# Kernel optimization log

Hardware: AMD Instinct MI355X
Metric: run time of the kernel (lower is better)

## Reference

```python
import jax, jax.numpy as jnp
import numpy as np

N = 100000   # nodes per type (author == paper count here)
E = 800000   # edges per edge type
D = 128      # input feature dim
HID = 128    # hidden_channels
OUT = 64     # out_channels
L = 2        # num_layers


def setup_inputs() -> dict:
    key = jax.random.key(0)
    ks = jax.random.split(key, 14)
    x_author = jax.random.normal(ks[0], (N, D), jnp.float32)
    x_paper = jax.random.normal(ks[1], (N, D), jnp.float32)
    edge_ap = jnp.stack([
        jax.random.randint(ks[2], (E,), 0, N),
        jax.random.randint(ks[3], (E,), 0, N),
    ]).astype(jnp.int32)  # [2,E] author->paper (src,dst)
    # paper->author: ensure every paper id appears as a source so the
    # meta-path conversion keeps all E edges (static shape under jit)
    pa_src = jnp.concatenate([jnp.arange(N), jax.random.randint(ks[4], (E - N,), 0, N)]).astype(jnp.int32)
    pa_dst = jax.random.randint(ks[5], (E,), 0, N).astype(jnp.int32)
    edge_pa = jnp.stack([pa_src, pa_dst])
    perm = jax.random.permutation(ks[6], N).astype(jnp.int32)  # DGI corruption
    s = 0.05
    # SAGEConv params: [layer, edge_type] with edge_type 0 = (author->paper), 1 = (paper->author)
    sage_Wl = jax.random.normal(ks[7], (L, 2, HID, D), jnp.float32) * s   # neighbor lin
    sage_Wr = jax.random.normal(ks[8], (L, 2, HID, D), jnp.float32) * s   # root lin
    sage_b = jnp.zeros((L, 2, HID), jnp.float32)
    # GATConv (heads=1) params
    gat_W = jax.random.normal(ks[9], (OUT, HID), jnp.float32) * s
    gat_att_src = jax.random.normal(ks[10], (OUT,), jnp.float32) * s
    gat_att_dst = jax.random.normal(ks[11], (OUT,), jnp.float32) * s
    gat_b = jnp.zeros((OUT,), jnp.float32)
    prelu_a = jnp.asarray(0.25, jnp.float32)
    return dict(x_author=x_author, x_paper=x_paper, sage_Wl=sage_Wl, sage_Wr=sage_Wr,
                sage_b=sage_b, gat_W=gat_W, gat_att_src=gat_att_src, gat_att_dst=gat_att_dst,
                gat_b=gat_b, prelu_a=prelu_a, edge_ap=edge_ap, edge_pa=edge_pa, perm=perm)


def _sage(x_src, x_dst, src, dst, Wl, Wr, b, n_dst):
    # SAGEConv: mean-aggregate neighbor feats, lin_l(agg) + lin_r(root) + bias
    agg = jax.ops.segment_sum(x_src[src], dst, num_segments=n_dst)       # [n_dst, D]
    cnt = jax.ops.segment_sum(jnp.ones((src.shape[0],), x_src.dtype), dst, num_segments=n_dst)
    mean = agg / jnp.maximum(cnt, 1.0)[:, None]
    return mean @ Wl.T + x_dst @ Wr.T + b


def _gat_prelu(feat, src, dst, W, a_src, a_dst, b, prelu_a, n):
    # GATConv heads=1 (self loops already appended by caller) + PReLU
    h = feat @ W.T                                                        # [n, OUT]
    e = jax.nn.leaky_relu((h @ a_src)[src] + (h @ a_dst)[dst], 0.2)       # [E']
    m = jax.ops.segment_max(e, dst, num_segments=n)
    ex = jnp.exp(e - m[dst])
    den = jax.ops.segment_sum(ex, dst, num_segments=n)
    coef = ex / den[dst]
    out = jax.ops.segment_sum(coef[:, None] * h[src], dst, num_segments=n) + b
    return jnp.where(out >= 0, out, prelu_a * out)


def reference(x_author, x_paper, sage_Wl, sage_Wr, sage_b, gat_W, gat_att_src,
              gat_att_dst, gat_b, prelu_a, edge_ap, edge_pa, perm):
    # Original loop feeds xx_dict into every layer, so only the LAST layer's
    # output survives; and only x_dict['author'] is consumed downstream.
    l = L - 1
    h_author = jax.nn.leaky_relu(
        _sage(x_paper, x_author, edge_pa[0], edge_pa[1],
              sage_Wl[l, 1], sage_Wr[l, 1], sage_b[l, 1], N), 0.01)
    # meta-path author->author edges (paper mapped via last-write paper->author dict)
    p2a = jnp.zeros((N,), jnp.int32).at[edge_pa[0]].set(edge_pa[1])
    self_loop = jnp.arange(N, dtype=jnp.int32)  # GATConv add_self_loops=True
    meta_src = jnp.concatenate([edge_ap[0], self_loop])
    meta_dst = jnp.concatenate([p2a[edge_ap[1]], self_loop])
    pos = _gat_prelu(h_author, meta_src, meta_dst, gat_W, gat_att_src, gat_att_dst, gat_b, prelu_a, N)
    neg = _gat_prelu(h_author[perm], meta_src, meta_dst, gat_W, gat_att_src, gat_att_dst, gat_b, prelu_a, N)
    summary = jnp.mean(pos, axis=0)
    return pos, neg, summary
```

## Files before the change

### kernel.cpp

```cpp
#include <hip/hip_runtime.h>
#include <stdint.h>

#define NN 100000
#define EE 800000
#define DD 128
#define HH 128
#define OO 64

#define SPA 40
#define SME 112
#define CPAD 16

typedef __attribute__((ext_vector_type(8))) short short8v;
typedef __attribute__((ext_vector_type(4))) float f32x4;

__device__ __forceinline__ unsigned short f2bf(float f) {
    union { float f; unsigned int u; } v; v.f = f;
    unsigned int u = v.u;
    u = (u + 0x7fffu + ((u >> 16) & 1u)) >> 16;
    return (unsigned short)u;
}
__device__ __forceinline__ float bf2f(unsigned short b) {
    union { unsigned int u; float f; } v; v.u = ((unsigned int)b) << 16;
    return v.f;
}

__global__ __launch_bounds__(256) void k_cast(const float* __restrict__ x,
                                              unsigned short* __restrict__ xbf) {
    long i = (long)blockIdx.x * 256 + threadIdx.x;
    if (i >= (long)NN * DD / 4) return;
    float4 v = ((const float4*)x)[i];
    ushort4 w;
    w.x = f2bf(v.x); w.y = f2bf(v.y); w.z = f2bf(v.z); w.w = f2bf(v.w);
    ((ushort4*)xbf)[i] = w;
}

__global__ __launch_bounds__(256) void k_p2a_init(const int* __restrict__ pa_dst,
                                                  unsigned long long* __restrict__ p2a) {
    int s = blockIdx.x * 256 + threadIdx.x;
    if (s >= NN) return;
    p2a[s] = ((unsigned long long)(unsigned int)s << 32) | (unsigned int)pa_dst[s];
}

__global__ __launch_bounds__(256) void k_p2a(const int* __restrict__ pa_src,
                                             const int* __restrict__ pa_dst,
                                             unsigned long long* __restrict__ p2a,
                                             int* __restrict__ cnt_pa,
                                             int* __restrict__ col_pa) {
    int e = blockIdx.x * 256 + threadIdx.x;
    if (e >= EE) return;
    int s = pa_src[e], d = pa_dst[e];
    if (e >= NN) {
        unsigned long long key = ((unsigned long long)(unsigned int)e << 32) | (unsigned int)d;
        atomicMax(&p2a[s], key);
    }
    int pos = atomicAdd(&cnt_pa[d * CPAD], 1);
    if (pos < SPA) __builtin_nontemporal_store(s, &col_pa[d * SPA + pos]);
}

__global__ __launch_bounds__(256) void k_compact(const unsigned long long* __restrict__ p2a,
                                                 int* __restrict__ p2a32) {
    int s = blockIdx.x * 256 + threadIdx.x;
    if (s >= NN) return;
    p2a32[s] = (int)(p2a[s] & 0xffffffffull);
}

__global__ __launch_bounds__(256) void k_meta(const int* __restrict__ ap_src,
                                              const int* __restrict__ ap_dst,
                                              const int* __restrict__ p2a32,
                                              int* __restrict__ cnt_meta,
                                              int* __restrict__ col_meta) {
    int e = blockIdx.x * 256 + threadIdx.x;
    if (e >= EE) return;
    int d = p2a32[ap_dst[e]];
    int pos = atomicAdd(&cnt_meta[d * CPAD], 1);
    if (pos < SME) __builtin_nontemporal_store(ap_src[e], &col_meta[d * SME + pos]);
}

__global__ __launch_bounds__(256) void k_sage_gather(const int* __restrict__ cnt_pa,
                                                     const int* __restrict__ col_pa,
                                                     const unsigned short* __restrict__ xbf,
                                                     unsigned short* __restrict__ mean_bf) {
    long gid = (long)blockIdx.x * 256 + threadIdx.x;
    int d = (int)(gid >> 6);
    if (d >= NN) return;
    int lane = (int)(gid & 63);
    int dcnt = cnt_pa[d * CPAD];
    int deg = (dcnt > SPA) ? SPA : dcnt;
    const int* row = col_pa + d * SPA;
    float ax = 0.f, ay = 0.f;
    int i = 0;
    for (; i + 3 < deg; i += 4) {
        int s0 = row[i], s1 = row[i + 1], s2 = row[i + 2], s3 = row[i + 3];
        ushort2 v0 = ((const ushort2*)(xbf + (long)s0 * DD))[lane];
        ushort2 v1 = ((const ushort2*)(xbf + (long)s1 * DD))[lane];
        ushort2 v2 = ((const ushort2*)(xbf + (long)s2 * DD))[lane];
        ushort2 v3 = ((const ushort2*)(xbf + (long)s3 * DD))[lane];
        ax += (bf2f(v0.x) + bf2f(v1.x)) + (bf2f(v2.x) + bf2f(v3.x));
        ay += (bf2f(v0.y) + bf2f(v1.y)) + (bf2f(v2.y) + bf2f(v3.y));
    }
    for (; i < deg; ++i) {
        int s = row[i];
        ushort2 v = ((const ushort2*)(xbf + (long)s * DD))[lane];
        ax += bf2f(v.x);
        ay += bf2f(v.y);
    }
    float sc = 1.0f / fmaxf((float)dcnt, 1.0f);
    ushort2 w;
    w.x = f2bf(ax * sc);
    w.y = f2bf(ay * sc);
    ((ushort2*)(mean_bf + (long)d * DD))[lane] = w;
}

__global__ __launch_bounds__(256) void k_sagegemm(const unsigned short* __restrict__ mean_bf,
                                                  const float* __restrict__ xa,
                                                  const float* __restrict__ Wl,
                                                  const float* __restrict__ Wr,
                                                  const float* __restrict__ sb,
                                                  unsigned short* __restrict__ h) {
    __shared__ unsigned short wlds[2][HH * DD];
    int t = threadIdx.x;
    #pragma unroll
    for (int it = 0; it < 8; ++it) {
        int cid = t + it * 256;
        int o = cid >> 4, c = cid & 15;
        int boff = (o * 256 + c * 16) ^ ((o & 7) << 4);
        {
            const float4* p = (const float4*)(Wl + (long)o * DD + c * 8);
            float4 a = p[0], b = p[1];
            short8v w;
            w[0]=(short)f2bf(a.x); w[1]=(short)f2bf(a.y); w[2]=(short)f2bf(a.z); w[3]=(short)f2bf(a.w);
            w[4]=(short)f2bf(b.x); w[5]=(short)f2bf(b.y); w[6]=(short)f2bf(b.z); w[7]=(short)f2bf(b.w);
            *(short8v*)((char*)(&wlds[0][0]) + boff) = w;
        }
        {
            const float4* p = (const float4*)(Wr + (long)o * DD + c * 8);
            float4 a = p[0], b = p[1];
            short8v w;
            w[0]=(short)f2bf(a.x); w[1]=(short)f2bf(a.y); w[2]=(short)f2bf(a.z); w[3]=(short)f2bf(a.w);
            w[4]=(short)f2bf(b.x); w[5]=(short)f2bf(b.y); w[6]=(short)f2bf(b.z); w[7]=(short)f2bf(b.w);
            *(short8v*)((char*)(&wlds[1][0]) + boff) = w;
        }
    }
    __syncthreads();

    int wave = t >> 6, lane = t & 63;
    int rowbase = blockIdx.x * 128 + wave * 32;
    int lr = lane & 15;
    int kq = (lane >> 4) * 8;
    int r0 = rowbase + lr, r1 = r0 + 16;
    int cr0 = (r0 < NN) ? r0 : 0;
    int cr1 = (r1 < NN) ? r1 : 0;

    f32x4 acc[2][8];
    #pragma unroll
    for (int i = 0; i < 2; ++i)
        #pragma unroll
        for (int j = 0; j < 8; ++j) { f32x4 z = {0.f,0.f,0.f,0.f}; acc[i][j] = z; }

    #pragma unroll
    for (int k0 = 0; k0 < DD; k0 += 32) {
        int kk = k0 + kq;
        short8v am0 = *(const short8v*)(mean_bf + (long)cr0 * DD + kk);
        short8v am1 = *(const short8v*)(mean_bf + (long)cr1 * DD + kk);
        const float4* q0 = (const float4*)(xa + (long)cr0 * DD + kk);
        const float4* q1 = (const float4*)(xa + (long)cr1 * DD + kk);
        float4 a0 = q0[0], b0 = q0[1], a1 = q1[0], b1 = q1[1];
        short8v ax0, ax1;
        ax0[0]=(short)f2bf(a0.x); ax0[1]=(short)f2bf(a0.y); ax0[2]=(short)f2bf(a0.z); ax0[3]=(short)f2bf(a0.w);
        ax0[4]=(short)f2bf(b0.x); ax0[5]=(short)f2bf(b0.y); ax0[6]=(short)f2bf(b0.z); ax0[7]=(short)f2bf(b0.w);
        ax1[0]=(short)f2bf(a1.x); ax1[1]=(short)f2bf(a1.y); ax1[2]=(short)f2bf(a1.z); ax1[3]=(short)f2bf(a1.w);
        ax1[4]=(short)f2bf(b1.x); ax1[5]=(short)f2bf(b1.y); ax1[6]=(short)f2bf(b1.z); ax1[7]=(short)f2bf(b1.w);
        #pragma unroll
        for (int nb = 0; nb < 8; ++nb) {
            int o = nb * 16 + lr;
            int boff = (o * 256 + kk * 2) ^ ((o & 7) << 4);
            short8v bl = *(const short8v*)((const char*)(&wlds[0][0]) + boff);
            short8v br = *(const short8v*)((const char*)(&wlds[1][0]) + boff);
            acc[0][nb] = __builtin_amdgcn_mfma_f32_16x16x32_bf16(am0, bl, acc[0][nb], 0, 0, 0);
            acc[1][nb] = __builtin_amdgcn_mfma_f32_16x16x32_bf16(am1, bl, acc[1][nb], 0, 0, 0);
            acc[0][nb] = __builtin_amdgcn_mfma_f32_16x16x32_bf16(ax0, br, acc[0][nb], 0, 0, 0);
            acc[1][nb] = __builtin_amdgcn_mfma_f32_16x16x32_bf16(ax1, br, acc[1][nb], 0, 0, 0);
        }
    }
    int q = lane >> 4;
    #pragma unroll
    for (int rh = 0; rh < 2; ++rh) {
        #pragma unroll
        for (int nb = 0; nb < 8; ++nb) {
            int col = nb * 16 + lr;
            float bias = sb[col];
            #pragma unroll
            for (int r = 0; r < 4; ++r) {
                int row = rowbase + rh * 16 + q * 4 + r;
                if (row < NN) {
                    float v = acc[rh][nb][r] + bias;
                    v = (v >= 0.f) ? v : 0.01f * v;
                    h[(long)row * HH + col] = f2bf(v);
                }
            }
        }
    }
}

__global__ __launch_bounds__(256) void k_gatgemm(const unsigned short* __restrict__ h,
                                                 const float* __restrict__ Wg,
                                                 const float* __restrict__ asrc,
                                                 const float* __restrict__ adst,
                                                 unsigned short* __restrict__ hg,
                                                 float* __restrict__ al_s,
                                                 float* __restrict__ al_d) {
    __shared__ unsigned short wlds[OO * HH];
    int t = threadIdx.x;
    #pragma unroll
    for (int it = 0; it < 4; ++it) {
        int cid = t + it * 256;
        int o = cid >> 4, c = cid & 15;
        int boff = (o * 256 + c * 16) ^ ((o & 7) << 4);
        const float4* p = (const float4*)(Wg + (long)o * HH + c * 8);
        float4 a = p[0], b = p[1];
        short8v w;
        w[0]=(short)f2bf(a.x); w[1]=(short)f2bf(a.y); w[2]=(short)f2bf(a.z); w[3]=(short)f2bf(a.w);
        w[4]=(short)f2bf(b.x); w[5]=(short)f2bf(b.y); w[6]=(short)f2bf(b.z); w[7]=(short)f2bf(b.w);
        *(short8v*)((char*)(&wlds[0]) + boff) = w;
    }
    __syncthreads();

    int wave = t >> 6, lane = t & 63;
    int rowbase = blockIdx.x * 128 + wave * 32;
    int lr = lane & 15;
    int kq = (lane >> 4) * 8;
    int r0 = rowbase + lr, r1 = r0 + 16;
    int cr0 = (r0 < NN) ? r0 : 0;
    int cr1 = (r1 < NN) ? r1 : 0;

    f32x4 acc[2][4];
    #pragma unroll
    for (int i = 0; i < 2; ++i)
        #pragma unroll
        for (int j = 0; j < 4; ++j) { f32x4 z = {0.f,0.f,0.f,0.f}; acc[i][j] = z; }

    #pragma unroll
    for (int k0 = 0; k0 < HH; k0 += 32) {
        int kk = k0 + kq;
        short8v a0 = *(const short8v*)(h + (long)cr0 * HH + kk);
        short8v a1 = *(const short8v*)(h + (long)cr1 * HH + kk);
        #pragma unroll
        for (int nb = 0; nb < 4; ++nb) {
            int o = nb * 16 + lr;
            int boff = (o * 256 + kk * 2) ^ ((o & 7) << 4);
            short8v b = *(const short8v*)((const char*)(&wlds[0]) + boff);
            acc[0][nb] = __builtin_amdgcn_mfma_f32_16x16x32_bf16(a0, b, acc[0][nb], 0, 0, 0);
            acc[1][nb] = __builtin_amdgcn_mfma_f32_16x16x32_bf16(a1, b, acc[1][nb], 0, 0, 0);
        }
    }
    int q = lane >> 4;
    float a_s[4], a_d[4];
    #pragma unroll
    for (int nb = 0; nb < 4; ++nb) { a_s[nb] = asrc[nb * 16 + lr]; a_d[nb] = adst[nb * 16 + lr]; }
    #pragma unroll
    for (int rh = 0; rh < 2; ++rh) {
        float ss[4] = {0.f,0.f,0.f,0.f}, dd[4] = {0.f,0.f,0.f,0.f};
        #pragma unroll
        for (int nb = 0; nb < 4; ++nb) {
            #pragma unroll
            for (int r = 0; r < 4; ++r) {
                int row = rowbase + rh * 16 + q * 4 + r;
                unsigned short wb = f2bf(acc[rh][nb][r]);
                if (row < NN) hg[(long)row * OO + nb * 16 + lr] = wb;
                float w = bf2f(wb);
                ss[r] += w * a_s[nb];
                dd[r] += w * a_d[nb];
            }
        }
        #pragma unroll
        for (int r = 0; r < 4; ++r) {
            float s = ss[r], dv = dd[r];
            #pragma unroll
            for (int off = 1; off < 16; off <<= 1) {
                s  += __shfl_xor(s,  off, 64);
                dv += __shfl_xor(dv, off, 64);
            }
            int row = rowbase + rh * 16 + q * 4 + r;
            if (lr == 0 && row < NN) { al_s[row] = s; al_d[row] = dv; }
        }
    }
}

__global__ __launch_bounds__(256) void k_gat_gather(const int* __restrict__ cnt_meta,
                                                    const int* __restrict__ col_meta,
                                                    const int* __restrict__ perm,
                                                    const float* __restrict__ al_s,
                                                    const float* __restrict__ al_d,
                                                    const unsigned short* __restrict__ hg,
                                                    const float* __restrict__ gb,
                                                    const float* __restrict__ prelu_a,
                                                    float* __restrict__ out) {
    long gid = (long)blockIdx.x * 256 + threadIdx.x;
    int d = (int)(gid >> 6);
    if (d >= NN) return;
    int j = (int)(gid & 63);
    int deg = cnt_meta[d * CPAD];
    if (deg > SME) deg = SME;
    const int* row = col_meta + d * SME;
    int pd = perm[d];
    float add = al_d[d];
    float adn = al_d[pd];
    float lp = al_s[d] + add;   lp = (lp >= 0.f) ? lp : 0.2f * lp;
    float ln = al_s[pd] + adn;  ln = (ln >= 0.f) ? ln : 0.2f * ln;
    float xps = __expf(lp), xns = __expf(ln);
    float denp = xps, denn = xns;
    float accp = xps * bf2f(hg[((long)d << 6) + j]);
    float accn = xns * bf2f(hg[((long)pd << 6) + j]);

    for (int base = 0; base < deg; base += 64) {
        int cnt = deg - base;
        if (cnt > 64) cnt = 64;
        int s = 0, ps = 0;
        float xp = 0.f, xn = 0.f;
        if (j < cnt) {
            s = row[base + j];
            ps = perm[s];
            float l0 = al_s[s] + add;   l0 = (l0 >= 0.f) ? l0 : 0.2f * l0;
            xp = __expf(l0);
            float m0 = al_s[ps] + adn;  m0 = (m0 >= 0.f) ? m0 : 0.2f * m0;
            xn = __expf(m0);
        }
        float tp = xp, tn = xn;
        #pragma unroll
        for (int off = 32; off; off >>= 1) {
            tp += __shfl_xor(tp, off, 64);
            tn += __shfl_xor(tn, off, 64);
        }
        denp += tp;
        denn += tn;
        int e = 0;
        for (; e + 3 < cnt; e += 4) {
            int s0 = __shfl(s, e),   s1 = __shfl(s, e + 1),   s2 = __shfl(s, e + 2),   s3 = __shfl(s, e + 3);
            int p0 = __shfl(ps, e),  p1 = __shfl(ps, e + 1),  p2 = __shfl(ps, e + 2),  p3 = __shfl(ps, e + 3);
            float a0 = __shfl(xp, e), a1 = __shfl(xp, e + 1), a2 = __shfl(xp, e + 2), a3 = __shfl(xp, e + 3);
            float b0 = __shfl(xn, e), b1 = __shfl(xn, e + 1), b2 = __shfl(xn, e + 2), b3 = __shfl(xn, e + 3);
            float h0 = bf2f(hg[((long)s0 << 6) + j]);
            float h1 = bf2f(hg[((long)s1 << 6) + j]);
            float h2 = bf2f(hg[((long)s2 << 6) + j]);
            float h3 = bf2f(hg[((long)s3 << 6) + j]);
            float g0 = bf2f(hg[((long)p0 << 6) + j]);
            float g1 = bf2f(hg[((long)p1 << 6) + j]);
            float g2 = bf2f(hg[((long)p2 << 6) + j]);
            float g3 = bf2f(hg[((long)p3 << 6) + j]);
            accp += (a0 * h0 + a1 * h1) + (a2 * h2 + a3 * h3);
            accn += (b0 * g0 + b1 * g1) + (b2 * g2 + b3 * g3);
        }
        for (; e < cnt; ++e) {
            int sb = __shfl(s, e);
            int pb = __shfl(ps, e);
            float ab = __shfl(xp, e);
            float bb = __shfl(xn, e);
            accp += ab * bf2f(hg[((long)sb << 6) + j]);
            accn += bb * bf2f(hg[((long)pb << 6) + j]);
        }
    }
    float bias = gb[j];
    float a = prelu_a[0];
    float vp = accp / denp + bias;
    vp = (vp >= 0.f) ? vp : a * vp;
    out[((long)d << 6) + j] = vp;
    float vn = accn / denn + bias;
    vn = (vn >= 0.f) ? vn : a * vn;
    out[((long)(NN + d) << 6) + j] = vn;
}

__global__ __launch_bounds__(256) void k_summary(const float* __restrict__ out_pos,
                                                 float* __restrict__ summary) {
    int t = threadIdx.x;
    int j = t & 63, sub = t >> 6;
    float acc = 0.f;
    for (int row = blockIdx.x * 4 + sub; row < NN; row += 256 * 4) {
        acc += out_pos[(long)row * OO + j];
    }
    __shared__ float red[4][OO];
    red[sub][j] = acc;
    __syncthreads();
    if (sub == 0) {
        float ttl = red[0][j] + red[1][j] + red[2][j] + red[3][j];
        atomicAdd(summary + j, ttl * (1.0f / NN));
    }
}

extern "C" void kernel_launch(void* const* d_in, const int* in_sizes, int n_in,
                              void* d_out, int out_size, void* d_ws, size_t ws_size,
                              hipStream_t stream) {
    const float* x_author = (const float*)d_in[0];
    const float* x_paper  = (const float*)d_in[1];
    const float* sage_Wl  = (const float*)d_in[2];
    const float* sage_Wr  = (const float*)d_in[3];
    const float* sage_b   = (const float*)d_in[4];
    const float* gat_W    = (const float*)d_in[5];
    const float* gat_as   = (const float*)d_in[6];
    const float* gat_ad   = (const float*)d_in[7];
    const float* gat_b    = (const float*)d_in[8];
    const float* prelu_a  = (const float*)d_in[9];
    const int*   edge_ap  = (const int*)d_in[10];
    const int*   edge_pa  = (const int*)d_in[11];
    const int*   perm     = (const int*)d_in[12];

    char* ws = (char*)d_ws;
    int*   cnt_pa    = (int*)(ws + 0);
    int*   cnt_meta  = (int*)(ws + 6400000);
    unsigned long long* p2a = (unsigned long long*)(ws + 12800000);
    int*   p2a32     = (int*)(ws + 13600000);
    float* al_s      = (float*)(ws + 14000000);
    float* al_d      = (float*)(ws + 14400000);
    int*   col_pa    = (int*)(ws + 14800000);
    unsigned short* xbf     = (unsigned short*)(ws + 30800000);
    unsigned short* mean_bf = (unsigned short*)(ws + 56400000);
    int*   col_meta  = (int*)(ws + 56400000);
    unsigned short* h  = xbf;
    unsigned short* hg = (unsigned short*)col_pa;

    hipMemsetAsync(d_ws, 0, 12800000, stream);
    hipMemsetAsync((char*)d_out + (size_t)2 * NN * OO * sizeof(float), 0,
                   OO * sizeof(float), stream);

    const float* Wl = sage_Wl + 3 * HH * DD;
    const float* Wr = sage_Wr + 3 * HH * DD;
    const float* sb = sage_b  + 3 * HH;

    k_cast<<<(NN * DD / 4 + 255) / 256, 256, 0, stream>>>(x_paper, xbf);
    k_p2a_init<<<(NN + 255) / 256, 256, 0, stream>>>(edge_pa + EE, p2a);
    k_p2a<<<(EE + 255) / 256, 256, 0, stream>>>(edge_pa, edge_pa + EE, p2a, cnt_pa, col_pa);
    k_compact<<<(NN + 255) / 256, 256, 0, stream>>>(p2a, p2a32);
    k_sage_gather<<<(NN * 64 + 255) / 256, 256, 0, stream>>>(cnt_pa, col_pa, xbf, mean_bf);
    k_sagegemm<<<(NN + 127) / 128, 256, 0, stream>>>(mean_bf, x_author, Wl, Wr, sb, h);
    k_gatgemm<<<(NN + 127) / 128, 256, 0, stream>>>(h, gat_W, gat_as, gat_ad, hg, al_s, al_d);
    k_meta<<<(EE + 255) / 256, 256, 0, stream>>>(edge_ap, edge_ap + EE, p2a32, cnt_meta, col_meta);
    k_gat_gather<<<(NN * 64 + 255) / 256, 256, 0, stream>>>(cnt_meta, col_meta, perm,
                                                            al_s, al_d, hg, gat_b, prelu_a,
                                                            (float*)d_out);
    k_summary<<<256, 256, 0, stream>>>((float*)d_out, (float*)d_out + 2L * NN * OO);
}
```

Before: 361.5 us.

## Fuse independent prep kernels via block-range dispatch and shrink counter padding

Independent stages now share one launch each, with the block index picking the role: edge CSR build, p2a seeding and the bf16 cast together; the SAGE gather with p2a compaction; the meta CSR build with the GAT GEMM. This cuts the launch count from ten to six. The last-write p2a map is now an int atomicMax on the edge index with a later lookup, replacing 64-bit packed keys. Counter padding (CPAD) is removed, which shrinks the memset but puts many counters on each cache line, so atomic contention on shared lines may rise.

```diff
diff --git a/kernel.cpp b/kernel.cpp
--- a/kernel.cpp
+++ b/kernel.cpp
@@ -9,7 +9,14 @@
 
 #define SPA 40
 #define SME 112
-#define CPAD 16
+
+#define PREP_EDGE_B 3125
+#define PREP_SEED_B 391
+#define PREP_CAST_B 12500
+#define P2_SAGE_B  25000
+#define P2_CMP_B   391
+#define P3_META_B  3125
+#define P3_GEMM_B  782
 
 typedef __attribute__((ext_vector_type(8))) short short8v;
 typedef __attribute__((ext_vector_type(4))) float f32x4;
@@ -25,91 +32,78 @@
     return v.f;
 }
 
-__global__ __launch_bounds__(256) void k_cast(const float* __restrict__ x,
+__global__ __launch_bounds__(256) void k_prep(const int* __restrict__ pa_src,
+                                              const int* __restrict__ pa_dst,
+                                              const float* __restrict__ x,
+                                              int* __restrict__ amax,
+                                              int* __restrict__ cnt_pa,
+                                              int* __restrict__ col_pa,
                                               unsigned short* __restrict__ xbf) {
-    long i = (long)blockIdx.x * 256 + threadIdx.x;
-    if (i >= (long)NN * DD / 4) return;
-    float4 v = ((const float4*)x)[i];
-    ushort4 w;
-    w.x = f2bf(v.x); w.y = f2bf(v.y); w.z = f2bf(v.z); w.w = f2bf(v.w);
-    ((ushort4*)xbf)[i] = w;
-}
-
-__global__ __launch_bounds__(256) void k_p2a_init(const int* __restrict__ pa_dst,
-                                                  unsigned long long* __restrict__ p2a) {
-    int s = blockIdx.x * 256 + threadIdx.x;
-    if (s >= NN) return;
-    p2a[s] = ((unsigned long long)(unsigned int)s << 32) | (unsigned int)pa_dst[s];
-}
-
-__global__ __launch_bounds__(256) void k_p2a(const int* __restrict__ pa_src,
-                                             const int* __restrict__ pa_dst,
-                                             unsigned long long* __restrict__ p2a,
-                                             int* __restrict__ cnt_pa,
-                                             int* __restrict__ col_pa) {
-    int e = blockIdx.x * 256 + threadIdx.x;
-    if (e >= EE) return;
-    int s = pa_src[e], d = pa_dst[e];
-    if (e >= NN) {
-        unsigned long long key = ((unsigned long long)(unsigned int)e << 32) | (unsigned int)d;
-        atomicMax(&p2a[s], key);
-    }
-    int pos = atomicAdd(&cnt_pa[d * CPAD], 1);
-    if (pos < SPA) __builtin_nontemporal_store(s, &col_pa[d * SPA + pos]);
-}
-
-__global__ __launch_bounds__(256) void k_compact(const unsigned long long* __restrict__ p2a,
-                                                 int* __restrict__ p2a32) {
-    int s = blockIdx.x * 256 + threadIdx.x;
-    if (s >= NN) return;
-    p2a32[s] = (int)(p2a[s] & 0xffffffffull);
-}
-
-__global__ __launch_bounds__(256) void k_meta(const int* __restrict__ ap_src,
-                                              const int* __restrict__ ap_dst,
-                                              const int* __restrict__ p2a32,
-                                              int* __restrict__ cnt_meta,
-                                              int* __restrict__ col_meta) {
-    int e = blockIdx.x * 256 + threadIdx.x;
-    if (e >= EE) return;
-    int d = p2a32[ap_dst[e]];
-    int pos = atomicAdd(&cnt_meta[d * CPAD], 1);
-    if (pos < SME) __builtin_nontemporal_store(ap_src[e], &col_meta[d * SME + pos]);
-}
-
-__global__ __launch_bounds__(256) void k_sage_gather(const int* __restrict__ cnt_pa,
-                                                     const int* __restrict__ col_pa,
-                                                     const unsigned short* __restrict__ xbf,
-                                                     unsigned short* __restrict__ mean_bf) {
-    long gid = (long)blockIdx.x * 256 + threadIdx.x;
-    int d = (int)(gid >> 6);
-    if (d >= NN) return;
-    int lane = (int)(gid & 63);
-    int dcnt = cnt_pa[d * CPAD];
-    int deg = (dcnt > SPA) ? SPA : dcnt;
-    const int* row = col_pa + d * SPA;
-    float ax = 0.f, ay = 0.f;
-    int i = 0;
-    for (; i + 3 < deg; i += 4) {
-        int s0 = row[i], s1 = row[i + 1], s2 = row[i + 2], s3 = row[i + 3];
-        ushort2 v0 = ((const ushort2*)(xbf + (long)s0 * DD))[lane];
-        ushort2 v1 = ((const ushort2*)(xbf + (long)s1 * DD))[lane];
-        ushort2 v2 = ((const ushort2*)(xbf + (long)s2 * DD))[lane];
-        ushort2 v3 = ((const ushort2*)(xbf + (long)s3 * DD))[lane];
-        ax += (bf2f(v0.x) + bf2f(v1.x)) + (bf2f(v2.x) + bf2f(v3.x));
-        ay += (bf2f(v0.y) + bf2f(v1.y)) + (bf2f(v2.y) + bf2f(v3.y));
-    }
-    for (; i < deg; ++i) {
-        int s = row[i];
-        ushort2 v = ((const ushort2*)(xbf + (long)s * DD))[lane];
-        ax += bf2f(v.x);
-        ay += bf2f(v.y);
-    }
-    float sc = 1.0f / fmaxf((float)dcnt, 1.0f);
-    ushort2 w;
-    w.x = f2bf(ax * sc);
-    w.y = f2bf(ay * sc);
-    ((ushort2*)(mean_bf + (long)d * DD))[lane] = w;
+    int b = blockIdx.x, t = threadIdx.x;
+    if (b < PREP_EDGE_B) {
+        int e = b * 256 + t;
+        if (e >= EE) return;
+        int s = pa_src[e], d = pa_dst[e];
+        if (e >= NN) atomicMax(&amax[s], e);
+        int pos = atomicAdd(&cnt_pa[d], 1);
+        if (pos < SPA) __builtin_nontemporal_store(s, &col_pa[d * SPA + pos]);
+    } else if (b < PREP_EDGE_B + PREP_SEED_B) {
+        int s = (b - PREP_EDGE_B) * 256 + t;
+        if (s >= NN) return;
+        atomicMax(&amax[s], s);
+    } else {
+        long i = (long)(b - PREP_EDGE_B - PREP_SEED_B) * 256 + t;
+        if (i >= (long)NN * DD / 4) return;
+        float4 v = ((const float4*)x)[i];
+        ushort4 w;
+        w.x = f2bf(v.x); w.y = f2bf(v.y); w.z = f2bf(v.z); w.w = f2bf(v.w);
+        ((ushort4*)xbf)[i] = w;
+    }
+}
+
+__global__ __launch_bounds__(256) void k_pack2(const int* __restrict__ cnt_pa,
+                                               const int* __restrict__ col_pa,
+                                               const unsigned short* __restrict__ xbf,
+                                               const int* __restrict__ amax,
+                                               const int* __restrict__ pa_dst,
+                                               int* __restrict__ p2a32,
+                                               unsigned short* __restrict__ mean_bf) {
+    int b = blockIdx.x, t = threadIdx.x;
+    if (b < P2_SAGE_B) {
+        long gid = (long)b * 256 + t;
+        int d = (int)(gid >> 6);
+        if (d >= NN) return;
+        int lane = (int)(gid & 63);
+        int dcnt = cnt_pa[d];
+        int deg = (dcnt > SPA) ? SPA : dcnt;
+        const int* row = col_pa + d * SPA;
+        float ax = 0.f, ay = 0.f;
+        int i = 0;
+        for (; i + 3 < deg; i += 4) {
+            int s0 = row[i], s1 = row[i + 1], s2 = row[i + 2], s3 = row[i + 3];
+            ushort2 v0 = ((const ushort2*)(xbf + (long)s0 * DD))[lane];
+            ushort2 v1 = ((const ushort2*)(xbf + (long)s1 * DD))[lane];
+            ushort2 v2 = ((const ushort2*)(xbf + (long)s2 * DD))[lane];
+            ushort2 v3 = ((const ushort2*)(xbf + (long)s3 * DD))[lane];
+            ax += (bf2f(v0.x) + bf2f(v1.x)) + (bf2f(v2.x) + bf2f(v3.x));
+            ay += (bf2f(v0.y) + bf2f(v1.y)) + (bf2f(v2.y) + bf2f(v3.y));
+        }
+        for (; i < deg; ++i) {
+            int s = row[i];
+            ushort2 v = ((const ushort2*)(xbf + (long)s * DD))[lane];
+            ax += bf2f(v.x);
+            ay += bf2f(v.y);
+        }
+        float sc = 1.0f / fmaxf((float)dcnt, 1.0f);
+        ushort2 w;
+        w.x = f2bf(ax * sc);
+        w.y = f2bf(ay * sc);
+        ((ushort2*)(mean_bf + (long)d * DD))[lane] = w;
+    } else {
+        int s = (b - P2_SAGE_B) * 256 + t;
+        if (s >= NN) return;
+        p2a32[s] = pa_dst[amax[s]];
+    }
 }
 
 __global__ __launch_bounds__(256) void k_sagegemm(const unsigned short* __restrict__ mean_bf,
@@ -203,31 +197,45 @@
     }
 }
 
-__global__ __launch_bounds__(256) void k_gatgemm(const unsigned short* __restrict__ h,
-                                                 const float* __restrict__ Wg,
-                                                 const float* __restrict__ asrc,
-                                                 const float* __restrict__ adst,
-                                                 unsigned short* __restrict__ hg,
-                                                 float* __restrict__ al_s,
-                                                 float* __restrict__ al_d) {
+__global__ __launch_bounds__(256) void k_pack3(const int* __restrict__ ap_src,
+                                               const int* __restrict__ ap_dst,
+                                               const int* __restrict__ p2a32,
+                                               int* __restrict__ cnt_meta,
+                                               int* __restrict__ col_meta,
+                                               const unsigned short* __restrict__ h,
+                                               const float* __restrict__ Wg,
+                                               const float* __restrict__ asrc,
+                                               const float* __restrict__ adst,
+                                               unsigned short* __restrict__ hg,
+                                               float* __restrict__ al_s,
+                                               float* __restrict__ al_d) {
     __shared__ unsigned short wlds[OO * HH];
-    int t = threadIdx.x;
+    int b = blockIdx.x, t = threadIdx.x;
+    if (b < P3_META_B) {
+        int e = b * 256 + t;
+        if (e >= EE) return;
+        int d = p2a32[ap_dst[e]];
+        int pos = atomicAdd(&cnt_meta[d], 1);
+        if (pos < SME) __builtin_nontemporal_store(ap_src[e], &col_meta[d * SME + pos]);
+        return;
+    }
+    int bb = b - P3_META_B;
     #pragma unroll
     for (int it = 0; it < 4; ++it) {
         int cid = t + it * 256;
         int o = cid >> 4, c = cid & 15;
         int boff = (o * 256 + c * 16) ^ ((o & 7) << 4);
         const float4* p = (const float4*)(Wg + (long)o * HH + c * 8);
-        float4 a = p[0], b = p[1];
+        float4 a = p[0], bv = p[1];
         short8v w;
         w[0]=(short)f2bf(a.x); w[1]=(short)f2bf(a.y); w[2]=(short)f2bf(a.z); w[3]=(short)f2bf(a.w);
-        w[4]=(short)f2bf(b.x); w[5]=(short)f2bf(b.y); w[6]=(short)f2bf(b.z); w[7]=(short)f2bf(b.w);
+        w[4]=(short)f2bf(bv.x); w[5]=(short)f2bf(bv.y); w[6]=(short)f2bf(bv.z); w[7]=(short)f2bf(bv.w);
         *(short8v*)((char*)(&wlds[0]) + boff) = w;
     }
     __syncthreads();
 
     int wave = t >> 6, lane = t & 63;
-    int rowbase = blockIdx.x * 128 + wave * 32;
+    int rowbase = bb * 128 + wave * 32;
     int lr = lane & 15;
     int kq = (lane >> 4) * 8;
     int r0 = rowbase + lr, r1 = r0 + 16;
@@ -249,9 +257,9 @@
         for (int nb = 0; nb < 4; ++nb) {
             int o = nb * 16 + lr;
             int boff = (o * 256 + kk * 2) ^ ((o & 7) << 4);
-            short8v b = *(const short8v*)((const char*)(&wlds[0]) + boff);
-            acc[0][nb] = __builtin_amdgcn_mfma_f32_16x16x32_bf16(a0, b, acc[0][nb], 0, 0, 0);
-            acc[1][nb] = __builtin_amdgcn_mfma_f32_16x16x32_bf16(a1, b, acc[1][nb], 0, 0, 0);
+            short8v bv = *(const short8v*)((const char*)(&wlds[0]) + boff);
+            acc[0][nb] = __builtin_amdgcn_mfma_f32_16x16x32_bf16(a0, bv, acc[0][nb], 0, 0, 0);
+            acc[1][nb] = __builtin_amdgcn_mfma_f32_16x16x32_bf16(a1, bv, acc[1][nb], 0, 0, 0);
         }
     }
     int q = lane >> 4;
@@ -300,7 +308,7 @@
     int d = (int)(gid >> 6);
     if (d >= NN) return;
     int j = (int)(gid & 63);
-    int deg = cnt_meta[d * CPAD];
+    int deg = cnt_meta[d];
     if (deg > SME) deg = SME;
     const int* row = col_meta + d * SME;
     int pd = perm[d];
@@ -406,19 +414,19 @@
 
     char* ws = (char*)d_ws;
     int*   cnt_pa    = (int*)(ws + 0);
-    int*   cnt_meta  = (int*)(ws + 6400000);
-    unsigned long long* p2a = (unsigned long long*)(ws + 12800000);
-    int*   p2a32     = (int*)(ws + 13600000);
-    float* al_s      = (float*)(ws + 14000000);
-    float* al_d      = (float*)(ws + 14400000);
-    int*   col_pa    = (int*)(ws + 14800000);
-    unsigned short* xbf     = (unsigned short*)(ws + 30800000);
-    unsigned short* mean_bf = (unsigned short*)(ws + 56400000);
-    int*   col_meta  = (int*)(ws + 56400000);
+    int*   cnt_meta  = (int*)(ws + 400000);
+    int*   amax      = (int*)(ws + 800000);
+    int*   p2a32     = (int*)(ws + 1200000);
+    float* al_s      = (float*)(ws + 1600000);
+    float* al_d      = (float*)(ws + 2000000);
+    int*   col_pa    = (int*)(ws + 2400000);
+    unsigned short* xbf     = (unsigned short*)(ws + 18400000);
+    unsigned short* mean_bf = (unsigned short*)(ws + 44000000);
+    int*   col_meta  = (int*)(ws + 44000000);
     unsigned short* h  = xbf;
     unsigned short* hg = (unsigned short*)col_pa;
 
-    hipMemsetAsync(d_ws, 0, 12800000, stream);
+    hipMemsetAsync(d_ws, 0, 1200000, stream);
     hipMemsetAsync((char*)d_out + (size_t)2 * NN * OO * sizeof(float), 0,
                    OO * sizeof(float), stream);
 
@@ -426,14 +434,14 @@
     const float* Wr = sage_Wr + 3 * HH * DD;
     const float* sb = sage_b  + 3 * HH;
 
-    k_cast<<<(NN * DD / 4 + 255) / 256, 256, 0, stream>>>(x_paper, xbf);
-    k_p2a_init<<<(NN + 255) / 256, 256, 0, stream>>>(edge_pa + EE, p2a);
-    k_p2a<<<(EE + 255) / 256, 256, 0, stream>>>(edge_pa, edge_pa + EE, p2a, cnt_pa, col_pa);
-    k_compact<<<(NN + 255) / 256, 256, 0, stream>>>(p2a, p2a32);
-    k_sage_gather<<<(NN * 64 + 255) / 256, 256, 0, stream>>>(cnt_pa, col_pa, xbf, mean_bf);
-    k_sagegemm<<<(NN + 127) / 128, 256, 0, stream>>>(mean_bf, x_author, Wl, Wr, sb, h);
-    k_gatgemm<<<(NN + 127) / 128, 256, 0, stream>>>(h, gat_W, gat_as, gat_ad, hg, al_s, al_d);
-    k_meta<<<(EE + 255) / 256, 256, 0, stream>>>(edge_ap, edge_ap + EE, p2a32, cnt_meta, col_meta);
+    k_prep<<<PREP_EDGE_B + PREP_SEED_B + PREP_CAST_B, 256, 0, stream>>>(
+        edge_pa, edge_pa + EE, x_paper, amax, cnt_pa, col_pa, xbf);
+    k_pack2<<<P2_SAGE_B + P2_CMP_B, 256, 0, stream>>>(
+        cnt_pa, col_pa, xbf, amax, edge_pa + EE, p2a32, mean_bf);
+    k_sagegemm<<<P3_GEMM_B, 256, 0, stream>>>(mean_bf, x_author, Wl, Wr, sb, h);
+    k_pack3<<<P3_META_B + P3_GEMM_B, 256, 0, stream>>>(
+        edge_ap, edge_ap + EE, p2a32, cnt_meta, col_meta,
+        h, gat_W, gat_as, gat_ad, hg, al_s, al_d);
     k_gat_gather<<<(NN * 64 + 255) / 256, 256, 0, stream>>>(cnt_meta, col_meta, perm,
                                                             al_s, al_d, hg, gat_b, prelu_a,
                                                             (float*)d_out);
```

After: 359.8 us. Within noise of the previous version (-0.5%).
